# Kernel optimization log

Hardware: AMD Instinct MI355X
Metric: run time of the kernel (lower is better)

The kernel has to match this reference:

```python
import jax, jax.numpy as jnp
import numpy as np
from jax import lax

N, C_IN, DIMS, NW, T, H, W = 8, 64, 64, 8, 16, 64, 64
BN_EPS = 1e-5


def setup_inputs() -> dict:
    key = jax.random.key(0)
    ks = jax.random.split(key, 10)
    # kaiming-ish scales
    w_scale = (2.0 / (C_IN * 27)) ** 0.5
    return {
        "x": jax.random.normal(ks[0], (N, C_IN, T, H, W), dtype=jnp.float32),
        "weights": jax.random.normal(ks[1], (NW, DIMS, C_IN, 3, 3, 3), dtype=jnp.float32) * w_scale,
        "biases": jax.random.normal(ks[2], (NW, DIMS), dtype=jnp.float32),
        "se_w1": jax.random.normal(ks[3], (16, C_IN, 5, 5), dtype=jnp.float32) * (2.0 / (C_IN * 25)) ** 0.5,
        "se_b1": jnp.zeros((16,), dtype=jnp.float32),
        "se_w2": jax.random.normal(ks[4], (32, 16, 5, 5), dtype=jnp.float32) * (2.0 / (16 * 25)) ** 0.5,
        "se_b2": jnp.zeros((32,), dtype=jnp.float32),
        "lin_w": jax.random.normal(ks[5], (NW, 32), dtype=jnp.float32) * (1.0 / 32) ** 0.5,
        "lin_b": jnp.zeros((NW,), dtype=jnp.float32),
        "bn_gamma": jnp.ones((DIMS,), dtype=jnp.float32),
        "bn_beta": jnp.zeros((DIMS,), dtype=jnp.float32),
        "epochs_num": 15,
    }


def _forward(x, weights, biases, se_w1, se_b1, se_w2, se_b2, lin_w, lin_b, bn_gamma, bn_beta, epochs_num):
    tau = 30.0 - 2.9 * epochs_num if epochs_num < 10 else 1.0
    # std over temporal axis (torch.std -> unbiased, ddof=1): [n, c, h, w]
    std_x = jnp.std(x, axis=2, ddof=1)
    # squeeze-expand attention branch
    dn2d = ("NCHW", "OIHW", "NCHW")
    h1 = lax.conv_general_dilated(std_x, se_w1, (1, 1), "VALID", dimension_numbers=dn2d)
    h1 = jax.nn.relu(h1 + se_b1[None, :, None, None])
    h2 = lax.conv_general_dilated(h1, se_w2, (1, 1), "VALID", dimension_numbers=dn2d)
    h2 = jax.nn.relu(h2 + se_b2[None, :, None, None])
    pooled = jnp.max(h2, axis=(2, 3))                      # [n, 32]
    logits = pooled @ lin_w.T + lin_b                       # [n, num_weights]
    phi = jax.nn.softmax(logits / tau, axis=1)
    # per-sample dynamic kernels / biases
    dyn_w = jnp.einsum("bn,ncidhw->bcidhw", phi, weights)   # [n, dims, c_in, 3,3,3]
    dyn_b = phi @ biases                                    # [n, dims]
    # grouped conv3d (groups = n) == per-sample conv3d via vmap
    dn3d = ("NCDHW", "OIDHW", "NCDHW")
    def one_conv(xi, wi):
        return lax.conv_general_dilated(xi[None], wi, (1, 1, 1), "SAME", dimension_numbers=dn3d)[0]
    y = jax.vmap(one_conv)(x, dyn_w)                        # [n, dims, t, h, w]
    y = y + dyn_b[:, :, None, None, None]
    # BatchNorm3d (training mode, batch stats, biased var)
    mean = jnp.mean(y, axis=(0, 2, 3, 4))
    var = jnp.var(y, axis=(0, 2, 3, 4))
    b = lambda v: v[None, :, None, None, None]
    y = (y - b(mean)) * b(bn_gamma) * lax.rsqrt(b(var) + BN_EPS) + b(bn_beta)
    return jax.nn.relu(y)


def reference(x, weights, biases, se_w1, se_b1, se_w2, se_b2, lin_w, lin_b, bn_gamma, bn_beta, epochs_num):
    return _forward(x, weights, biases, se_w1, se_b1, se_w2, se_b2, lin_w, lin_b, bn_gamma, bn_beta, epochs_num)
```

## Files before the change

kernel.cpp:

```cpp
#include <hip/hip_runtime.h>
#include <hip/hip_bf16.h>
#include <math.h>

#define N_   8
#define CIN_ 64
#define DIMS_ 64
#define NW_  8
#define T_   16
#define H_   64
#define W_   64
#define HW_  (H_ * W_)
#define THW_ (T_ * HW_)

typedef short bf16x8 __attribute__((ext_vector_type(8)));
typedef float f32x16 __attribute__((ext_vector_type(16)));

__device__ __forceinline__ unsigned short f2bf(float f) {
    union { float f; unsigned u; } a; a.f = f;
    unsigned r = a.u + 0x7fffu + ((a.u >> 16) & 1u);
    return (unsigned short)(r >> 16);
}

#define CS8_ 8
#define HS8_ (66 * CS8_)
#define TS8_ (10 * HS8_)
#define XSH_ (3 * TS8_)
#define WLH_ (28 * 64 * 8)

__host__ __device__ constexpr int OXc(int tap) {
    int tt = tap > 26 ? 26 : tap;
    return (tt / 9) * TS8_ + ((tt % 9) / 3) * HS8_ + ((tt % 3) - 1) * CS8_;
}

__global__ __launch_bounds__(512) void stdxb_kernel(
    const float* __restrict__ x, float* __restrict__ std_x,
    unsigned short* __restrict__ xb, float* __restrict__ sums,
    unsigned* __restrict__ pooled)
{
    __shared__ unsigned short xsl[16 * 64 * 8];
    const int h = blockIdx.x, c8 = blockIdx.y, n = blockIdx.z;
    const int tid = threadIdx.x;
    if ((blockIdx.x | blockIdx.y | blockIdx.z) == 0) {
        if (tid < 128) sums[tid] = 0.f;
        else if (tid < 384) pooled[tid - 128] = 0u;
    }
    const int c = tid >> 6, w = tid & 63;
    const int cin = c8 * 8 + c;
    const float* px = x + (((size_t)(n * 64 + cin)) << 16) + (h << 6) + w;
    float s = 0.f, s2 = 0.f;
#pragma unroll
    for (int t = 0; t < T_; ++t) {
        float v = px[t * HW_];
        s += v;
        s2 += v * v;
        xsl[(t << 9) + (w << 3) + c] = f2bf(v);
    }
    float var = (s2 - s * s * (1.0f / 16.0f)) * (1.0f / 15.0f);
    std_x[(((size_t)(n * 64 + cin)) << 12) + (h << 6) + w] = sqrtf(fmaxf(var, 0.f));
    __syncthreads();
    const int4* src = (const int4*)xsl;
    int4* dst = (int4*)(xb + ((size_t)((n * 8 + c8) * 16) << 12) * 8);
#pragma unroll
    for (int k = 0; k < 2; ++k) {
        int j = tid + (k << 9);
        int t = j >> 6, ww = j & 63;
        dst[((t << 6) + h) * 64 + ww] = src[j];
    }
}

__global__ void wtrans(const float* __restrict__ w1, const float* __restrict__ w2,
                       float* __restrict__ w1t, float* __restrict__ w2t) {
    int i = blockIdx.x * 256 + threadIdx.x;
    if (i < 25600) {
        int k = i / 1600, c = (i / 25) % 64, tap = i % 25;
        w1t[(c * 25 + tap) * 16 + k] = w1[i];
    } else if (i < 38400) {
        int j = i - 25600;
        int o = j / 400, c = (j / 25) % 16, tap = j % 25;
        w2t[(c * 25 + tap) * 32 + o] = w2[j];
    }
}

__global__ __launch_bounds__(256) void se_conv1c(const float* __restrict__ std_x,
        const float* __restrict__ w1t, const float* __restrict__ b1, float* __restrict__ h1) {
    __shared__ float red[3][64][8];
    const int n = blockIdx.y, ks = blockIdx.z * 8;
    const int iq = threadIdx.x & 63, cq = threadIdx.x >> 6;
    const int ij = blockIdx.x * 64 + iq;
    float acc[8];
#pragma unroll
    for (int q = 0; q < 8; ++q) acc[q] = 0.f;
    if (ij < 3600) {
        int i = ij / 60, j = ij - i * 60;
        const float* xn = std_x + (size_t)n * CIN_ * HW_ + i * W_ + j;
        for (int c = cq * 16; c < cq * 16 + 16; ++c) {
            const float* xc = xn + c * HW_;
            float xv[25];
#pragma unroll
            for (int u = 0; u < 5; ++u)
#pragma unroll
                for (int v = 0; v < 5; ++v) xv[u * 5 + v] = xc[u * W_ + v];
            const float* wc = w1t + c * 400 + ks;
#pragma unroll
            for (int tap = 0; tap < 25; ++tap)
#pragma unroll
                for (int q = 0; q < 8; ++q)
                    acc[q] = fmaf(xv[tap], wc[tap * 16 + q], acc[q]);
        }
    }
    if (cq > 0) {
#pragma unroll
        for (int q = 0; q < 8; ++q) red[cq - 1][iq][q] = acc[q];
    }
    __syncthreads();
    if (cq == 0 && ij < 3600) {
#pragma unroll
        for (int q = 0; q < 8; ++q) {
            float a = acc[q] + red[0][iq][q] + red[1][iq][q] + red[2][iq][q] + b1[ks + q];
            h1[((size_t)(n * 16 + ks + q)) * 3600 + ij] = fmaxf(a, 0.f);
        }
    }
}

__global__ __launch_bounds__(256) void se_conv2c(const float* __restrict__ h1,
        const float* __restrict__ w2t, const float* __restrict__ b2,
        unsigned* __restrict__ pooled) {
    __shared__ float red[3][64][8];
    const int n = blockIdx.y, os = blockIdx.z * 8;
    const int iq = threadIdx.x & 63, cq = threadIdx.x >> 6;
    const int ij = blockIdx.x * 64 + iq;
    const int i = ij / 56, j = ij - i * 56;
    float acc[8];
#pragma unroll
    for (int q = 0; q < 8; ++q) acc[q] = 0.f;
    const float* xn = h1 + (size_t)n * 16 * 3600 + i * 60 + j;
    for (int c = cq * 4; c < cq * 4 + 4; ++c) {
        const float* xc = xn + c * 3600;
        float xv[25];
#pragma unroll
        for (int u = 0; u < 5; ++u)
#pragma unroll
            for (int v = 0; v < 5; ++v) xv[u * 5 + v] = xc[u * 60 + v];
        const float* wc = w2t + c * 800 + os;
#pragma unroll
        for (int tap = 0; tap < 25; ++tap)
#pragma unroll
            for (int q = 0; q < 8; ++q)
                acc[q] = fmaf(xv[tap], wc[tap * 32 + q], acc[q]);
    }
    if (cq > 0) {
#pragma unroll
        for (int q = 0; q < 8; ++q) red[cq - 1][iq][q] = acc[q];
    }
    __syncthreads();
    if (cq == 0) {
#pragma unroll
        for (int q = 0; q < 8; ++q) {
            float a = fmaxf(acc[q] + red[0][iq][q] + red[1][iq][q] + red[2][iq][q] + b2[os + q], 0.f);
#pragma unroll
            for (int m = 1; m < 64; m <<= 1) a = fmaxf(a, __shfl_xor(a, m, 64));
            if (iq == 0) atomicMax(&pooled[n * 32 + os + q], __float_as_uint(a));
        }
    }
}

__global__ __launch_bounds__(256) void dyn_w_head(
    const float* __restrict__ weights, const float* __restrict__ pooled,
    const float* __restrict__ lin_w, const float* __restrict__ lin_b,
    const float* __restrict__ biases, const int* __restrict__ epochs,
    unsigned short* __restrict__ wtb2, float* __restrict__ dyn_b) {
    __shared__ float slog[8][8];
    __shared__ float sphi[64];
    const int tid = threadIdx.x;
    const int e = epochs[0];
    const float tau = (e < 10) ? (30.0f - 2.9f * (float)e) : 1.0f;
    if (tid < 64) {
        int b = tid >> 3, m = tid & 7;
        float acc = lin_b[m];
#pragma unroll
        for (int k = 0; k < 32; ++k) acc += pooled[b * 32 + k] * lin_w[m * 32 + k];
        slog[b][m] = acc / tau;
    }
    __syncthreads();
    if (tid < 8) {
        float mx = slog[tid][0];
#pragma unroll
        for (int m = 1; m < 8; ++m) mx = fmaxf(mx, slog[tid][m]);
        float ex[8], ssum = 0.f;
#pragma unroll
        for (int m = 0; m < 8; ++m) { ex[m] = expf(slog[tid][m] - mx); ssum += ex[m]; }
        float inv = 1.0f / ssum;
#pragma unroll
        for (int m = 0; m < 8; ++m) sphi[tid * 8 + m] = ex[m] * inv;
    }
    __syncthreads();
    if (blockIdx.x < 64) {
        int b = blockIdx.x >> 3, c8 = blockIdx.x & 7;
        unsigned* dst = (unsigned*)(wtb2 + (size_t)b * 114688 + (size_t)(c8 * 28 + 27) * 512);
        dst[tid] = 0u;
    }
    if (blockIdx.x == 0) {
#pragma unroll
        for (int idx = tid; idx < 512; idx += 256) {
            int b = idx >> 6, d = idx & 63;
            float a = 0.f;
#pragma unroll
            for (int m = 0; m < 8; ++m) a += sphi[b * 8 + m] * biases[m * DIMS_ + d];
            dyn_b[idx] = a;
        }
    }
    int f = blockIdx.x * 256 + tid;
    if (f >= 110592) return;
    int tap = f % 27, cin = (f / 27) & 63, co = f / 1728;
    float wv[8];
#pragma unroll
    for (int m = 0; m < 8; ++m) wv[m] = weights[(size_t)m * 110592 + f];
    size_t dbase = (size_t)(cin >> 3) * 14336 + tap * 512 + co * 8 + (cin & 7);
#pragma unroll
    for (int b = 0; b < 8; ++b) {
        float acc = 0.f;
#pragma unroll
        for (int m = 0; m < 8; ++m) acc += sphi[b * 8 + m] * wv[m];
        wtb2[(size_t)b * 114688 + dbase] = f2bf(acc);
    }
}

__global__ __launch_bounds__(256, 2) void conv3d_mfma5(
    const unsigned short* __restrict__ xb,
    const unsigned short* __restrict__ wtb2,
    const float* __restrict__ dynb,
    float* __restrict__ y,
    float* __restrict__ sums)
{
    __shared__ __align__(16) unsigned short xs[XSH_];
    __shared__ __align__(16) unsigned short wl[WLH_];
    __shared__ float bnred[128];

    const int hb = blockIdx.x, t = blockIdx.y, n = blockIdx.z;
    const int tid = threadIdx.x;
    const int lane = tid & 63, wid = tid >> 6;
    const int lane31 = lane & 31, tau = lane >> 5;
    const int hbase = hb * 8;

    for (int i = tid; i < XSH_ / 8; i += 256)
        *(int4*)&xs[i * 8] = (int4){0, 0, 0, 0};
    if (tid < 128) bnred[tid] = 0.f;

    const unsigned short* xnb = xb + (size_t)n * 4194304;
    const unsigned short* wnb = wtb2 + (size_t)n * 114688;

    f32x16 acc[2][4];
#pragma unroll
    for (int ci = 0; ci < 2; ++ci)
#pragma unroll
        for (int s = 0; s < 4; ++s)
            acc[ci][s] = (f32x16)(0.f);

    const int aBase = tau * 512 + lane31 * 8;
    int bsp[4];
#pragma unroll
    for (int s = 0; s < 4; ++s)
        bsp[s] = (2 * wid + (s >> 1)) * HS8_ + (1 + (s & 1) * 32 + lane31) * CS8_;

    for (int c8 = 0; c8 < 8; ++c8) {
        __syncthreads();
#pragma unroll
        for (int k = 0; k < 7; ++k) {
            int tp = wid + (k << 2);
            const unsigned short* gp = wnb + ((size_t)c8 * 14336 + tp * 512 + lane * 8);
            const unsigned short* lp = &wl[tp * 512];
            __builtin_amdgcn_global_load_lds(
                (const __attribute__((address_space(1))) void*)gp,
                (__attribute__((address_space(3))) void*)lp, 16, 0, 0);
        }
#pragma unroll
        for (int k = 0; k < 8; ++k) {
            int r = wid + (k << 2);
            if (r < 30) {
                int tp = (r >= 20) ? 2 : (r >= 10 ? 1 : 0);
                int hp = r - tp * 10;
                int gt = t + tp - 1, gh = hbase + hp - 1;
                if (((unsigned)gt < 16u) && ((unsigned)gh < 64u)) {
                    const unsigned short* gp = xnb + (size_t)(((c8 * 16 + gt) * 64 + gh) * 64 + lane) * 8;
                    const unsigned short* lp = &xs[tp * TS8_ + hp * HS8_ + CS8_];
                    __builtin_amdgcn_global_load_lds(
                        (const __attribute__((address_space(1))) void*)gp,
                        (__attribute__((address_space(3))) void*)lp, 16, 0, 0);
                }
            }
        }
        __syncthreads();

#pragma unroll
        for (int p = 0; p < 14; ++p) {
            const int xo = tau ? OXc(2 * p + 1) : OXc(2 * p);
            bf16x8 a0 = *(const bf16x8*)&wl[p * 1024 + aBase];
            bf16x8 a1 = *(const bf16x8*)&wl[p * 1024 + aBase + 256];
            bf16x8 b0 = *(const bf16x8*)&xs[bsp[0] + xo];
            bf16x8 b1 = *(const bf16x8*)&xs[bsp[1] + xo];
            bf16x8 b2 = *(const bf16x8*)&xs[bsp[2] + xo];
            bf16x8 b3 = *(const bf16x8*)&xs[bsp[3] + xo];
            acc[0][0] = __builtin_amdgcn_mfma_f32_32x32x16_bf16(a0, b0, acc[0][0], 0, 0, 0);
            acc[0][1] = __builtin_amdgcn_mfma_f32_32x32x16_bf16(a0, b1, acc[0][1], 0, 0, 0);
            acc[0][2] = __builtin_amdgcn_mfma_f32_32x32x16_bf16(a0, b2, acc[0][2], 0, 0, 0);
            acc[0][3] = __builtin_amdgcn_mfma_f32_32x32x16_bf16(a0, b3, acc[0][3], 0, 0, 0);
            acc[1][0] = __builtin_amdgcn_mfma_f32_32x32x16_bf16(a1, b0, acc[1][0], 0, 0, 0);
            acc[1][1] = __builtin_amdgcn_mfma_f32_32x32x16_bf16(a1, b1, acc[1][1], 0, 0, 0);
            acc[1][2] = __builtin_amdgcn_mfma_f32_32x32x16_bf16(a1, b2, acc[1][2], 0, 0, 0);
            acc[1][3] = __builtin_amdgcn_mfma_f32_32x32x16_bf16(a1, b3, acc[1][3], 0, 0, 0);
        }
    }

    const float* db = dynb + n * DIMS_;
#pragma unroll
    for (int ci = 0; ci < 2; ++ci) {
#pragma unroll
        for (int r = 0; r < 16; ++r) {
            const int co = 32 * ci + (r & 3) + 8 * (r >> 2) + 4 * tau;
            const float bco = db[co];
            float ps = 0.f, ps2 = 0.f;
#pragma unroll
            for (int s = 0; s < 4; ++s) {
                float z = acc[ci][s][r] + bco;
                size_t yi = ((size_t)(n * 64 + co) << 16) + ((size_t)t << 12)
                          + ((size_t)(hbase + 2 * wid + (s >> 1)) << 6) + (s & 1) * 32 + lane31;
                y[yi] = z;
                ps += z;
                ps2 += z * z;
            }
#pragma unroll
            for (int m = 1; m < 32; m <<= 1) {
                ps += __shfl_xor(ps, m, 64);
                ps2 += __shfl_xor(ps2, m, 64);
            }
            if (lane31 == 0) {
                atomicAdd(&bnred[co], ps);
                atomicAdd(&bnred[64 + co], ps2);
            }
        }
    }
    __syncthreads();
    if (tid < 128) atomicAdd(&sums[tid], bnred[tid]);
}

__global__ void bn_norm4(const float* __restrict__ sums, const float* __restrict__ gamma,
                         const float* __restrict__ beta, float* __restrict__ y) {
    const float cnt = (float)(N_ * THW_);
    for (size_t idx = (size_t)blockIdx.x * 256 + threadIdx.x; idx < 8388608;
         idx += (size_t)4096 * 256) {
        int c = (int)((idx >> 14) & 63);
        float mean = sums[c] / cnt;
        float var = sums[64 + c] / cnt - mean * mean;
        float sc = gamma[c] * rsqrtf(var + 1e-5f);
        float sh = beta[c] - mean * sc;
        float4 v = ((float4*)y)[idx];
        v.x = fmaxf(fmaf(v.x, sc, sh), 0.f);
        v.y = fmaxf(fmaf(v.y, sc, sh), 0.f);
        v.z = fmaxf(fmaf(v.z, sc, sh), 0.f);
        v.w = fmaxf(fmaf(v.w, sc, sh), 0.f);
        ((float4*)y)[idx] = v;
    }
}

extern "C" void kernel_launch(void* const* d_in, const int* in_sizes, int n_in,
                              void* d_out, int out_size, void* d_ws, size_t ws_size,
                              hipStream_t stream) {
    const float* x       = (const float*)d_in[0];
    const float* weights = (const float*)d_in[1];
    const float* biases  = (const float*)d_in[2];
    const float* se_w1   = (const float*)d_in[3];
    const float* se_b1   = (const float*)d_in[4];
    const float* se_w2   = (const float*)d_in[5];
    const float* se_b2   = (const float*)d_in[6];
    const float* lin_w   = (const float*)d_in[7];
    const float* lin_b   = (const float*)d_in[8];
    const float* gamma   = (const float*)d_in[9];
    const float* beta    = (const float*)d_in[10];
    const int*   epochs  = (const int*)d_in[11];

    float* out = (float*)d_out;
    float* ws = (float*)d_ws;

    const size_t STD_OFF  = 0;
    const size_t H1_OFF   = STD_OFF + 2097152;
    const size_t SUMS_OFF = H1_OFF + 460800;
    const size_t POOL_OFF = SUMS_OFF + 128;
    const size_t PHI_OFF  = POOL_OFF + 256;
    const size_t DYNB_OFF = PHI_OFF + 64;
    const size_t WTB_OFF  = DYNB_OFF + 512;
    const size_t W1T_OFF  = WTB_OFF + 458752;
    const size_t W2T_OFF  = W1T_OFF + 25600;
    const size_t XB_OFF   = W2T_OFF + 12800;

    float* std_x  = ws + STD_OFF;
    float* h1     = ws + H1_OFF;
    float* sums   = ws + SUMS_OFF;
    float* pooled = ws + POOL_OFF;
    float* dynb   = ws + DYNB_OFF;
    unsigned short* wtb2 = (unsigned short*)(ws + WTB_OFF);
    float* w1t    = ws + W1T_OFF;
    float* w2t    = ws + W2T_OFF;
    unsigned short* xb = (unsigned short*)(ws + XB_OFF);

    stdxb_kernel<<<dim3(64, 8, 8), 512, 0, stream>>>(x, std_x, xb, sums, (unsigned*)pooled);
    wtrans<<<150, 256, 0, stream>>>(se_w1, se_w2, w1t, w2t);

    se_conv1c<<<dim3(57, 8, 2), 256, 0, stream>>>(std_x, w1t, se_b1, h1);
    se_conv2c<<<dim3(49, 8, 4), 256, 0, stream>>>(h1, w2t, se_b2, (unsigned*)pooled);

    dyn_w_head<<<432, 256, 0, stream>>>(weights, pooled, lin_w, lin_b, biases, epochs,
                                        wtb2, dynb);

    conv3d_mfma5<<<dim3(8, 16, 8), 256, 0, stream>>>(xb, wtb2, dynb, out, sums);

    bn_norm4<<<4096, 256, 0, stream>>>(sums, gamma, beta, out);
}
```

Measured before the change: 372.2 us.

## Store pre-BN conv output in bf16, fold weight transpose, split SE conv outputs finer

When the workspace is large enough, the conv3d kernel writes its pre-normalization output as bf16 into a scratch buffer, and a new BN kernel reads bf16 and writes fp32 output. This halves the intermediate write and re-read traffic. The SE weight-transpose kernel is folded into the std/xb kernel to drop one launch. The SE conv kernels now compute 4 output channels per block instead of 8, doubling the grid for more parallelism. The bf16 intermediate adds rounding error before normalization, and the new path only runs if the workspace check passes.

```diff
diff --git a/kernel.cpp b/kernel.cpp
--- a/kernel.cpp
+++ b/kernel.cpp
@@ -20,6 +20,9 @@
     unsigned r = a.u + 0x7fffu + ((a.u >> 16) & 1u);
     return (unsigned short)(r >> 16);
 }
+__device__ __forceinline__ float bf2f(unsigned short u) {
+    union { unsigned u; float f; } a; a.u = ((unsigned)u) << 16; return a.f;
+}
 
 #define CS8_ 8
 #define HS8_ (66 * CS8_)
@@ -35,14 +38,28 @@
 __global__ __launch_bounds__(512) void stdxb_kernel(
     const float* __restrict__ x, float* __restrict__ std_x,
     unsigned short* __restrict__ xb, float* __restrict__ sums,
-    unsigned* __restrict__ pooled)
+    unsigned* __restrict__ pooled,
+    const float* __restrict__ w1, const float* __restrict__ w2,
+    float* __restrict__ w1t, float* __restrict__ w2t)
 {
     __shared__ unsigned short xsl[16 * 64 * 8];
     const int h = blockIdx.x, c8 = blockIdx.y, n = blockIdx.z;
     const int tid = threadIdx.x;
-    if ((blockIdx.x | blockIdx.y | blockIdx.z) == 0) {
+    const int bf = blockIdx.x + (blockIdx.y << 6) + ((int)blockIdx.z << 9);
+    if (bf == 0) {
         if (tid < 128) sums[tid] = 0.f;
         else if (tid < 384) pooled[tid - 128] = 0u;
+    }
+    if (bf < 75) {
+        int i = bf * 512 + tid;
+        if (i < 25600) {
+            int k = i / 1600, c = (i / 25) % 64, tap = i % 25;
+            w1t[(c * 25 + tap) * 16 + k] = w1[i];
+        } else if (i < 38400) {
+            int j = i - 25600;
+            int o = j / 400, c = (j / 25) % 16, tap = j % 25;
+            w2t[(c * 25 + tap) * 32 + o] = w2[j];
+        }
     }
     const int c = tid >> 6, w = tid & 63;
     const int cin = c8 * 8 + c;
@@ -68,28 +85,15 @@
     }
 }
 
-__global__ void wtrans(const float* __restrict__ w1, const float* __restrict__ w2,
-                       float* __restrict__ w1t, float* __restrict__ w2t) {
-    int i = blockIdx.x * 256 + threadIdx.x;
-    if (i < 25600) {
-        int k = i / 1600, c = (i / 25) % 64, tap = i % 25;
-        w1t[(c * 25 + tap) * 16 + k] = w1[i];
-    } else if (i < 38400) {
-        int j = i - 25600;
-        int o = j / 400, c = (j / 25) % 16, tap = j % 25;
-        w2t[(c * 25 + tap) * 32 + o] = w2[j];
-    }
-}
-
 __global__ __launch_bounds__(256) void se_conv1c(const float* __restrict__ std_x,
         const float* __restrict__ w1t, const float* __restrict__ b1, float* __restrict__ h1) {
-    __shared__ float red[3][64][8];
-    const int n = blockIdx.y, ks = blockIdx.z * 8;
+    __shared__ float red[3][64][4];
+    const int n = blockIdx.y, ks = blockIdx.z * 4;
     const int iq = threadIdx.x & 63, cq = threadIdx.x >> 6;
     const int ij = blockIdx.x * 64 + iq;
-    float acc[8];
-#pragma unroll
-    for (int q = 0; q < 8; ++q) acc[q] = 0.f;
+    float acc[4];
+#pragma unroll
+    for (int q = 0; q < 4; ++q) acc[q] = 0.f;
     if (ij < 3600) {
         int i = ij / 60, j = ij - i * 60;
         const float* xn = std_x + (size_t)n * CIN_ * HW_ + i * W_ + j;
@@ -104,18 +108,18 @@
 #pragma unroll
             for (int tap = 0; tap < 25; ++tap)
 #pragma unroll
-                for (int q = 0; q < 8; ++q)
+                for (int q = 0; q < 4; ++q)
                     acc[q] = fmaf(xv[tap], wc[tap * 16 + q], acc[q]);
         }
     }
     if (cq > 0) {
 #pragma unroll
-        for (int q = 0; q < 8; ++q) red[cq - 1][iq][q] = acc[q];
+        for (int q = 0; q < 4; ++q) red[cq - 1][iq][q] = acc[q];
     }
     __syncthreads();
     if (cq == 0 && ij < 3600) {
 #pragma unroll
-        for (int q = 0; q < 8; ++q) {
+        for (int q = 0; q < 4; ++q) {
             float a = acc[q] + red[0][iq][q] + red[1][iq][q] + red[2][iq][q] + b1[ks + q];
             h1[((size_t)(n * 16 + ks + q)) * 3600 + ij] = fmaxf(a, 0.f);
         }
@@ -125,14 +129,14 @@
 __global__ __launch_bounds__(256) void se_conv2c(const float* __restrict__ h1,
         const float* __restrict__ w2t, const float* __restrict__ b2,
         unsigned* __restrict__ pooled) {
-    __shared__ float red[3][64][8];
-    const int n = blockIdx.y, os = blockIdx.z * 8;
+    __shared__ float red[3][64][4];
+    const int n = blockIdx.y, os = blockIdx.z * 4;
     const int iq = threadIdx.x & 63, cq = threadIdx.x >> 6;
     const int ij = blockIdx.x * 64 + iq;
     const int i = ij / 56, j = ij - i * 56;
-    float acc[8];
-#pragma unroll
-    for (int q = 0; q < 8; ++q) acc[q] = 0.f;
+    float acc[4];
+#pragma unroll
+    for (int q = 0; q < 4; ++q) acc[q] = 0.f;
     const float* xn = h1 + (size_t)n * 16 * 3600 + i * 60 + j;
     for (int c = cq * 4; c < cq * 4 + 4; ++c) {
         const float* xc = xn + c * 3600;
@@ -145,17 +149,17 @@
 #pragma unroll
         for (int tap = 0; tap < 25; ++tap)
 #pragma unroll
-            for (int q = 0; q < 8; ++q)
+            for (int q = 0; q < 4; ++q)
                 acc[q] = fmaf(xv[tap], wc[tap * 32 + q], acc[q]);
     }
     if (cq > 0) {
 #pragma unroll
-        for (int q = 0; q < 8; ++q) red[cq - 1][iq][q] = acc[q];
+        for (int q = 0; q < 4; ++q) red[cq - 1][iq][q] = acc[q];
     }
     __syncthreads();
     if (cq == 0) {
 #pragma unroll
-        for (int q = 0; q < 8; ++q) {
+        for (int q = 0; q < 4; ++q) {
             float a = fmaxf(acc[q] + red[0][iq][q] + red[1][iq][q] + red[2][iq][q] + b2[os + q], 0.f);
 #pragma unroll
             for (int m = 1; m < 64; m <<= 1) a = fmaxf(a, __shfl_xor(a, m, 64));
@@ -230,6 +234,7 @@
     const unsigned short* __restrict__ wtb2,
     const float* __restrict__ dynb,
     float* __restrict__ y,
+    unsigned short* __restrict__ ybf,
     float* __restrict__ sums)
 {
     __shared__ __align__(16) unsigned short xs[XSH_];
@@ -312,6 +317,7 @@
     }
 
     const float* db = dynb + n * DIMS_;
+    const bool bf = (ybf != nullptr);
 #pragma unroll
     for (int ci = 0; ci < 2; ++ci) {
 #pragma unroll
@@ -324,7 +330,8 @@
                 float z = acc[ci][s][r] + bco;
                 size_t yi = ((size_t)(n * 64 + co) << 16) + ((size_t)t << 12)
                           + ((size_t)(hbase + 2 * wid + (s >> 1)) << 6) + (s & 1) * 32 + lane31;
-                y[yi] = z;
+                if (bf) ybf[yi] = f2bf(z);
+                else    y[yi] = z;
                 ps += z;
                 ps2 += z * z;
             }
@@ -341,6 +348,33 @@
     }
     __syncthreads();
     if (tid < 128) atomicAdd(&sums[tid], bnred[tid]);
+}
+
+__global__ void bn_norm_bf(const float* __restrict__ sums, const float* __restrict__ gamma,
+                           const float* __restrict__ beta,
+                           const unsigned short* __restrict__ ybf, float* __restrict__ out) {
+    const float cnt = (float)(N_ * THW_);
+    for (size_t i8 = (size_t)blockIdx.x * 256 + threadIdx.x; i8 < 4194304;
+         i8 += (size_t)4096 * 256) {
+        int c = (int)((i8 >> 13) & 63);
+        float mean = sums[c] / cnt;
+        float var = sums[64 + c] / cnt - mean * mean;
+        float sc = gamma[c] * rsqrtf(var + 1e-5f);
+        float sh = beta[c] - mean * sc;
+        int4 raw = ((const int4*)ybf)[i8];
+        const unsigned short* u = (const unsigned short*)&raw;
+        float4 o0, o1;
+        o0.x = fmaxf(fmaf(bf2f(u[0]), sc, sh), 0.f);
+        o0.y = fmaxf(fmaf(bf2f(u[1]), sc, sh), 0.f);
+        o0.z = fmaxf(fmaf(bf2f(u[2]), sc, sh), 0.f);
+        o0.w = fmaxf(fmaf(bf2f(u[3]), sc, sh), 0.f);
+        o1.x = fmaxf(fmaf(bf2f(u[4]), sc, sh), 0.f);
+        o1.y = fmaxf(fmaf(bf2f(u[5]), sc, sh), 0.f);
+        o1.z = fmaxf(fmaf(bf2f(u[6]), sc, sh), 0.f);
+        o1.w = fmaxf(fmaf(bf2f(u[7]), sc, sh), 0.f);
+        ((float4*)out)[i8 * 2]     = o0;
+        ((float4*)out)[i8 * 2 + 1] = o1;
+    }
 }
 
 __global__ void bn_norm4(const float* __restrict__ sums, const float* __restrict__ gamma,
@@ -391,6 +425,8 @@
     const size_t W1T_OFF  = WTB_OFF + 458752;
     const size_t W2T_OFF  = W1T_OFF + 25600;
     const size_t XB_OFF   = W2T_OFF + 12800;
+    const size_t YBF_OFF  = XB_OFF + 16777216;
+    const size_t NEEDED   = (YBF_OFF + 16777216) * 4;
 
     float* std_x  = ws + STD_OFF;
     float* h1     = ws + H1_OFF;
@@ -401,17 +437,24 @@
     float* w1t    = ws + W1T_OFF;
     float* w2t    = ws + W2T_OFF;
     unsigned short* xb = (unsigned short*)(ws + XB_OFF);
-
-    stdxb_kernel<<<dim3(64, 8, 8), 512, 0, stream>>>(x, std_x, xb, sums, (unsigned*)pooled);
-    wtrans<<<150, 256, 0, stream>>>(se_w1, se_w2, w1t, w2t);
-
-    se_conv1c<<<dim3(57, 8, 2), 256, 0, stream>>>(std_x, w1t, se_b1, h1);
-    se_conv2c<<<dim3(49, 8, 4), 256, 0, stream>>>(h1, w2t, se_b2, (unsigned*)pooled);
+    unsigned short* ybf = (unsigned short*)(ws + YBF_OFF);
+
+    const bool bf_path = (ws_size >= NEEDED);
+
+    stdxb_kernel<<<dim3(64, 8, 8), 512, 0, stream>>>(
+        x, std_x, xb, sums, (unsigned*)pooled, se_w1, se_w2, w1t, w2t);
+
+    se_conv1c<<<dim3(57, 8, 4), 256, 0, stream>>>(std_x, w1t, se_b1, h1);
+    se_conv2c<<<dim3(49, 8, 8), 256, 0, stream>>>(h1, w2t, se_b2, (unsigned*)pooled);
 
     dyn_w_head<<<432, 256, 0, stream>>>(weights, pooled, lin_w, lin_b, biases, epochs,
                                         wtb2, dynb);
 
-    conv3d_mfma5<<<dim3(8, 16, 8), 256, 0, stream>>>(xb, wtb2, dynb, out, sums);
-
-    bn_norm4<<<4096, 256, 0, stream>>>(sums, gamma, beta, out);
-}
+    conv3d_mfma5<<<dim3(8, 16, 8), 256, 0, stream>>>(
+        xb, wtb2, dynb, out, bf_path ? ybf : nullptr, sums);
+
+    if (bf_path)
+        bn_norm_bf<<<4096, 256, 0, stream>>>(sums, gamma, beta, ybf, out);
+    else
+        bn_norm4<<<4096, 256, 0, stream>>>(sums, gamma, beta, out);
+}
```

New measurement: 378.5 us. No clear change (+1.7%).
